# Performance work log

Hardware: AMD Instinct MI355X
Metric: run time of the kernel (lower is better)

## Reference

```python
import jax, jax.numpy as jnp
import numpy as np

N_SAMPLES = 8_388_608   # total packed samples (~64 per ray on average)
N_RAYS = 131_072
DT_SCALE = 0.005        # keep per-ray optical depth ~O(1); also tempers global-cumsum fp32 error


def setup_inputs() -> dict:
    key = jax.random.key(0)
    k1, k2, k3, k4, k5 = jax.random.split(key, 5)
    rgb_samples = jax.random.uniform(k1, (N_SAMPLES, 3), dtype=jnp.float32)
    radiance_samples = jax.random.uniform(k2, (N_SAMPLES, 1), dtype=jnp.float32)  # density sigma >= 0
    samples_z = jax.random.uniform(k3, (N_SAMPLES,), dtype=jnp.float32)           # t values in [0,1)
    samples_dt = jax.random.uniform(k4, (N_SAMPLES,), dtype=jnp.float32) * DT_SCALE
    # sorted segment ids == contiguous packed per-ray sample ranges (ragged)
    ray_id = jnp.sort(jax.random.randint(k5, (N_SAMPLES,), 0, N_RAYS, dtype=jnp.int64))
    ray_t_exit = jnp.full((N_RAYS, 1), 2.0, dtype=jnp.float32)  # exit t beyond all z -> positive last dt
    return {
        "rgb_samples": rgb_samples,
        "radiance_samples": radiance_samples,
        "samples_z": samples_z,
        "samples_dt": samples_dt,
        "ray_id": ray_id,
        "ray_t_exit": ray_t_exit,
        "use_ray_t_exit": 1,
    }


def reference(rgb_samples, radiance_samples, samples_z, samples_dt, ray_id, ray_t_exit, use_ray_t_exit):
    N = rgb_samples.shape[0]
    sigma = radiance_samples[:, 0]
    idx = jnp.arange(N)

    # dt of the last sample of each ray is (t_exit - z_last) when use_ray_t_exit
    if use_ray_t_exit:
        last_idx = jax.ops.segment_max(idx, ray_id, num_segments=N_RAYS)
        is_last = idx == last_idx[ray_id]
        dt = jnp.where(is_last, ray_t_exit[ray_id, 0] - samples_z, samples_dt)
    else:
        dt = samples_dt

    sigdt = sigma * dt                      # optical depth per sample
    c = jnp.cumsum(sigdt)                   # global inclusive cumsum
    c_excl = c - sigdt                      # global exclusive cumsum
    # exclusive cumsum restarted per ray: subtract value at each segment's first sample
    # (c_excl is non-decreasing since sigdt >= 0, so segment_min == first element)
    seg_start = jax.ops.segment_min(c_excl, ray_id, num_segments=N_RAYS)
    T = jnp.exp(-(c_excl - seg_start[ray_id]))          # transmittance before each sample
    alpha = 1.0 - jnp.exp(-sigdt)
    w = alpha * T                                        # per-sample compositing weight

    pred_rgb = jax.ops.segment_sum(w[:, None] * rgb_samples, ray_id, num_segments=N_RAYS)   # [R,3]
    pred_depth = jax.ops.segment_sum(w * samples_z, ray_id, num_segments=N_RAYS)[:, None]   # [R,1]
    bg_transmittance = jnp.exp(-jax.ops.segment_sum(sigdt, ray_id, num_segments=N_RAYS))[:, None]  # [R,1]
    weight_per_sample = w[:, None]                                                           # [N,1]
    return pred_rgb, pred_depth, bg_transmittance, weight_per_sample
```

## Files before the change

kernel.cpp:

```cpp
#include <hip/hip_runtime.h>


#define RPW 4

struct F2 { float x, y; };
struct F6 { float v[6]; };

template <int CTRL, int ROW_MASK>
__device__ __forceinline__ float dpp_add(float x) {
    int t = __builtin_amdgcn_update_dpp(0, __float_as_int(x), CTRL, ROW_MASK, 0xf, true);
    return x + __int_as_float(t);
}

__device__ __forceinline__ float wave_incl_scan(float x) {
    x = dpp_add<0x111, 0xf>(x);
    x = dpp_add<0x112, 0xf>(x);
    x = dpp_add<0x114, 0xf>(x);
    x = dpp_add<0x118, 0xf>(x);
    x = dpp_add<0x142, 0xa>(x);
    x = dpp_add<0x143, 0xc>(x);
    return x;
}

__device__ __forceinline__ float readlane_f32(float x, int lane) {
    return __int_as_float(__builtin_amdgcn_readlane(__float_as_int(x), lane));
}

__global__ void compute_starts_kernel(const int* __restrict__ ray_id,
                                      int n_samples, int n_rays,
                                      int* __restrict__ starts) {
    const int t = blockIdx.x * blockDim.x + threadIdx.x;
    const int stride = gridDim.x * blockDim.x;
    if (t == 0) {
        const int first = ray_id[0];
        for (int r = 0; r <= first; ++r) starts[r] = 0;
        const int last = ray_id[n_samples - 1];
        for (int r = last + 1; r <= n_rays; ++r) starts[r] = n_samples;
    }
    for (int g = t; g * 4 < n_samples; g += stride) {
        const int i4 = g * 4;
        const int4 v = *reinterpret_cast<const int4*>(ray_id + i4);
        const int prev = (i4 == 0) ? v.x : ray_id[i4 - 1];
        const int vals[5] = {prev, v.x, v.y, v.z, v.w};
        #pragma unroll
        for (int j = 0; j < 4; ++j) {
            const int p = vals[j], c = vals[j + 1];
            if (c != p) {
                for (int r = p + 1; r <= c; ++r) starts[r] = i4 + j;
            }
        }
    }
}

struct Slab { F2 sg, zv, dtv; F6 c; };

__device__ __forceinline__ Slab load_slab(const float* __restrict__ sigma_in,
                                          const float* __restrict__ z_in,
                                          const float* __restrict__ dt_in,
                                          const float* __restrict__ rgb,
                                          int base, int lane, int n_samples)
{
    Slab r;
    const int i0 = base + 2 * lane;
    const int il = min(i0, n_samples - 2);
    r.sg  = *reinterpret_cast<const F2*>(sigma_in + il);
    r.zv  = *reinterpret_cast<const F2*>(z_in + il);
    r.dtv = *reinterpret_cast<const F2*>(dt_in + il);
    r.c   = *reinterpret_cast<const F6*>(rgb + 3 * (size_t)il);
    if (i0 > n_samples - 2) {
        r.sg.x = r.sg.y; r.zv.x = r.zv.y; r.dtv.x = r.dtv.y;
        r.c.v[0] = r.c.v[3]; r.c.v[1] = r.c.v[4]; r.c.v[2] = r.c.v[5];
    }
    return r;
}

__device__ __forceinline__ void process_pass128(
    const Slab& d, int base, int s1, int lane, int use_exit, float texit,
    float& csum, float& carry,
    float& accR, float& accG, float& accB, float& accD,
    float* __restrict__ out_w)
{
    const int i0 = base + 2 * lane;
    const int i1 = i0 + 1;
    float dt0 = d.dtv.x, dt1v = d.dtv.y;
    if (use_exit && i0 == s1 - 1) dt0  = texit - d.zv.x;
    if (use_exit && i1 == s1 - 1) dt1v = texit - d.zv.y;
    const float e0 = (i0 < s1) ? d.sg.x * dt0  : 0.f;
    const float e1 = (i1 < s1) ? d.sg.y * dt1v : 0.f;

    const float S  = wave_incl_scan(e0 + e1);
    const float t1 = csum + S;
    const float t0 = t1 - e1;
    const float v0 = __expf(-t0);
    const float v1 = __expf(-t1);
    const int vpi = __builtin_amdgcn_update_dpp(__float_as_int(carry), __float_as_int(v1),
                                                0x138 , 0xf, 0xf, false);
    const float vp = __int_as_float(vpi);
    const float w0 = vp - v0;
    const float w1 = v0 - v1;

    if (i0 < s1) out_w[i0] = w0;
    if (i1 < s1) out_w[i1] = w1;
    accR += w0 * d.c.v[0] + w1 * d.c.v[3];
    accG += w0 * d.c.v[1] + w1 * d.c.v[4];
    accB += w0 * d.c.v[2] + w1 * d.c.v[5];
    accD += w0 * d.zv.x   + w1 * d.zv.y;
    csum  = readlane_f32(t1, 63);
    carry = readlane_f32(v1, 63);
}

__global__ __launch_bounds__(256) void render_kernel(
    const float* __restrict__ rgb,
    const float* __restrict__ sigma_in,
    const float* __restrict__ z_in,
    const float* __restrict__ dt_in,
    const float* __restrict__ t_exit,
    const int*  __restrict__ use_exit_p,
    const int*  __restrict__ starts,
    float* __restrict__ out_rgb,
    float* __restrict__ out_depth,
    float* __restrict__ out_bg,
    float* __restrict__ out_w,
    int n_rays, int n_samples)
{
    const int wave = threadIdx.x >> 6;
    const int lane = threadIdx.x & 63;
    const int wid  = blockIdx.x * (blockDim.x >> 6) + wave;
    const int ray0 = wid * RPW;
    if (ray0 >= n_rays) return;

    const int use_exit = *use_exit_p;

    int s[RPW + 1];
    #pragma unroll
    for (int k = 0; k <= RPW; ++k) {
        s[k] = __builtin_amdgcn_readfirstlane(starts[min(ray0 + k, n_rays)]);
    }
    float texit[RPW];
    #pragma unroll
    for (int k = 0; k < RPW; ++k) {
        texit[k] = readlane_f32(t_exit[min(ray0 + k, n_rays - 1)], 0);
    }

    Slab sl[RPW];
    #pragma unroll
    for (int k = 0; k < RPW; ++k) {
        sl[k] = load_slab(sigma_in, z_in, dt_in, rgb, s[k], lane, n_samples);
    }
    #pragma unroll
    for (int k = 0; k < RPW; ++k) {
        asm volatile("" ::
            "v"(sl[k].sg.x), "v"(sl[k].sg.y), "v"(sl[k].zv.x), "v"(sl[k].zv.y),
            "v"(sl[k].dtv.x), "v"(sl[k].dtv.y),
            "v"(sl[k].c.v[0]), "v"(sl[k].c.v[1]), "v"(sl[k].c.v[2]),
            "v"(sl[k].c.v[3]), "v"(sl[k].c.v[4]), "v"(sl[k].c.v[5]));
    }
    __builtin_amdgcn_sched_barrier(0);

    #pragma unroll
    for (int k = 0; k < RPW; ++k) {
        const int ray = ray0 + k;
        if (ray >= n_rays) break;
        const int s0 = s[k], s1 = s[k + 1];
        float csum = 0.f, carry = 1.0f;
        float accR = 0.f, accG = 0.f, accB = 0.f, accD = 0.f;

        process_pass128(sl[k], s0, s1, lane, use_exit, texit[k],
                        csum, carry, accR, accG, accB, accD, out_w);

        for (int base = s0 + 128; base < s1; base += 128) {
            const Slab d = load_slab(sigma_in, z_in, dt_in, rgb, base, lane, n_samples);
            process_pass128(d, base, s1, lane, use_exit, texit[k],
                            csum, carry, accR, accG, accB, accD, out_w);
        }

        accR = wave_incl_scan(accR);
        accG = wave_incl_scan(accG);
        accB = wave_incl_scan(accB);
        accD = wave_incl_scan(accD);
        if (lane == 63) {
            out_rgb[3 * ray + 0] = accR;
            out_rgb[3 * ray + 1] = accB == accB ? accG : accG;
            out_rgb[3 * ray + 1] = accG;
            out_rgb[3 * ray + 2] = accB;
            out_depth[ray] = accD;
            out_bg[ray]    = carry;
        }
    }
}

extern "C" void kernel_launch(void* const* d_in, const int* in_sizes, int n_in,
                              void* d_out, int out_size, void* d_ws, size_t ws_size,
                              hipStream_t stream) {
    const float* rgb     = (const float*)d_in[0];
    const float* sigma   = (const float*)d_in[1];
    const float* z       = (const float*)d_in[2];
    const float* dt      = (const float*)d_in[3];
    const int*   ray_id  = (const int*)d_in[4];
    const float* t_exit  = (const float*)d_in[5];
    const int*   use_ex  = (const int*)d_in[6];

    const int n_samples = in_sizes[2];
    const int n_rays    = in_sizes[5];

    int* starts = (int*)d_ws;

    float* out      = (float*)d_out;
    float* out_rgb  = out;
    float* out_dep  = out + (size_t)3 * n_rays;
    float* out_bg   = out + (size_t)4 * n_rays;
    float* out_w    = out + (size_t)5 * n_rays;

    compute_starts_kernel<<<2048, 256, 0, stream>>>(ray_id, n_samples, n_rays, starts);

    const int waves_per_block = 4;
    const int rays_per_block  = waves_per_block * RPW;
    const int blocks = (n_rays + rays_per_block - 1) / rays_per_block;
    render_kernel<<<blocks, 256, 0, stream>>>(rgb, sigma, z, dt, t_exit, use_ex,
                                              starts, out_rgb, out_dep, out_bg,
                                              out_w, n_rays, n_samples);
}
```

Before: 58.56 us.

## Interleave first-pass scans across rays and split rare long-ray continuation path

Computes the first 128-sample pass for all four rays of a wave as independent unrolled chains, so their DPP scans and exps can interleave instead of running serially per ray. Rays longer than 128 samples are handled in a separate wave-uniform branch that resumes from the saved prefix and carry. The first-pass weight stores and the final per-ray reductions are batched after that branch. It also drops the early return and the asm register pinning. Keeping more values live raises register pressure, and removing the early exit makes out-of-range waves run the full body.

```diff
diff --git a/kernel.cpp b/kernel.cpp
--- a/kernel.cpp
+++ b/kernel.cpp
@@ -74,37 +74,31 @@
     return r;
 }
 
-__device__ __forceinline__ void process_pass128(
+__device__ __forceinline__ void process_pass128_rare(
     const Slab& d, int base, int s1, int lane, int use_exit, float texit,
     float& csum, float& carry,
-    float& accR, float& accG, float& accB, float& accD,
+    float& aR, float& aG, float& aB, float& aD,
     float* __restrict__ out_w)
 {
-    const int i0 = base + 2 * lane;
-    const int i1 = i0 + 1;
-    float dt0 = d.dtv.x, dt1v = d.dtv.y;
-    if (use_exit && i0 == s1 - 1) dt0  = texit - d.zv.x;
-    if (use_exit && i1 == s1 - 1) dt1v = texit - d.zv.y;
-    const float e0 = (i0 < s1) ? d.sg.x * dt0  : 0.f;
-    const float e1 = (i1 < s1) ? d.sg.y * dt1v : 0.f;
-
-    const float S  = wave_incl_scan(e0 + e1);
-    const float t1 = csum + S;
-    const float t0 = t1 - e1;
-    const float v0 = __expf(-t0);
+    const int i0 = base + 2 * lane, i1 = i0 + 1;
+    float dt0 = d.dtv.x, dt1 = d.dtv.y;
+    if (use_exit && i0 == s1 - 1) dt0 = texit - d.zv.x;
+    if (use_exit && i1 == s1 - 1) dt1 = texit - d.zv.y;
+    const float e0 = (i0 < s1) ? d.sg.x * dt0 : 0.f;
+    const float e1 = (i1 < s1) ? d.sg.y * dt1 : 0.f;
+    const float t1 = csum + wave_incl_scan(e0 + e1);
+    const float v0 = __expf(-(t1 - e1));
     const float v1 = __expf(-t1);
     const int vpi = __builtin_amdgcn_update_dpp(__float_as_int(carry), __float_as_int(v1),
                                                 0x138 , 0xf, 0xf, false);
-    const float vp = __int_as_float(vpi);
-    const float w0 = vp - v0;
+    const float w0 = __int_as_float(vpi) - v0;
     const float w1 = v0 - v1;
-
     if (i0 < s1) out_w[i0] = w0;
     if (i1 < s1) out_w[i1] = w1;
-    accR += w0 * d.c.v[0] + w1 * d.c.v[3];
-    accG += w0 * d.c.v[1] + w1 * d.c.v[4];
-    accB += w0 * d.c.v[2] + w1 * d.c.v[5];
-    accD += w0 * d.zv.x   + w1 * d.zv.y;
+    aR += w0 * d.c.v[0] + w1 * d.c.v[3];
+    aG += w0 * d.c.v[1] + w1 * d.c.v[4];
+    aB += w0 * d.c.v[2] + w1 * d.c.v[5];
+    aD += w0 * d.zv.x + w1 * d.zv.y;
     csum  = readlane_f32(t1, 63);
     carry = readlane_f32(v1, 63);
 }
@@ -127,7 +121,6 @@
     const int lane = threadIdx.x & 63;
     const int wid  = blockIdx.x * (blockDim.x >> 6) + wave;
     const int ray0 = wid * RPW;
-    if (ray0 >= n_rays) return;
 
     const int use_exit = *use_exit_p;
 
@@ -136,10 +129,10 @@
     for (int k = 0; k <= RPW; ++k) {
         s[k] = __builtin_amdgcn_readfirstlane(starts[min(ray0 + k, n_rays)]);
     }
-    float texit[RPW];
-    #pragma unroll
-    for (int k = 0; k < RPW; ++k) {
-        texit[k] = readlane_f32(t_exit[min(ray0 + k, n_rays - 1)], 0);
+    float tex[RPW];
+    #pragma unroll
+    for (int k = 0; k < RPW; ++k) {
+        tex[k] = readlane_f32(t_exit[min(ray0 + k, n_rays - 1)], 0);
     }
 
     Slab sl[RPW];
@@ -147,44 +140,74 @@
     for (int k = 0; k < RPW; ++k) {
         sl[k] = load_slab(sigma_in, z_in, dt_in, rgb, s[k], lane, n_samples);
     }
-    #pragma unroll
-    for (int k = 0; k < RPW; ++k) {
-        asm volatile("" ::
-            "v"(sl[k].sg.x), "v"(sl[k].sg.y), "v"(sl[k].zv.x), "v"(sl[k].zv.y),
-            "v"(sl[k].dtv.x), "v"(sl[k].dtv.y),
-            "v"(sl[k].c.v[0]), "v"(sl[k].c.v[1]), "v"(sl[k].c.v[2]),
-            "v"(sl[k].c.v[3]), "v"(sl[k].c.v[4]), "v"(sl[k].c.v[5]));
-    }
     __builtin_amdgcn_sched_barrier(0);
 
-    #pragma unroll
-    for (int k = 0; k < RPW; ++k) {
+    float accR[RPW], accG[RPW], accB[RPW], accD[RPW];
+    float w0v[RPW], w1v[RPW], t1v[RPW], v1v[RPW];
+    #pragma unroll
+    for (int k = 0; k < RPW; ++k) {
+        const int s1 = s[k + 1];
+        const int i0 = s[k] + 2 * lane;
+        const int i1 = i0 + 1;
+        float dt0 = sl[k].dtv.x, dt1 = sl[k].dtv.y;
+        if (use_exit && i0 == s1 - 1) dt0 = tex[k] - sl[k].zv.x;
+        if (use_exit && i1 == s1 - 1) dt1 = tex[k] - sl[k].zv.y;
+        const float e0 = (i0 < s1) ? sl[k].sg.x * dt0 : 0.f;
+        const float e1 = (i1 < s1) ? sl[k].sg.y * dt1 : 0.f;
+        const float t1 = wave_incl_scan(e0 + e1);
+        const float v0 = __expf(-(t1 - e1));
+        const float v1 = __expf(-t1);
+        const int vpi = __builtin_amdgcn_update_dpp(0x3f800000 , __float_as_int(v1),
+                                                    0x138 , 0xf, 0xf, false);
+        const float vp = __int_as_float(vpi);
+        const float w0 = vp - v0;
+        const float w1 = v0 - v1;
+        w0v[k] = w0;  w1v[k] = w1;
+        accR[k] = w0 * sl[k].c.v[0] + w1 * sl[k].c.v[3];
+        accG[k] = w0 * sl[k].c.v[1] + w1 * sl[k].c.v[4];
+        accB[k] = w0 * sl[k].c.v[2] + w1 * sl[k].c.v[5];
+        accD[k] = w0 * sl[k].zv.x   + w1 * sl[k].zv.y;
+        t1v[k] = t1;  v1v[k] = v1;
+    }
+
+    bool anylong = false;
+    #pragma unroll
+    for (int k = 0; k < RPW; ++k) anylong |= (s[k] + 128 < s[k + 1]);
+    if (anylong) {
+        #pragma unroll
+        for (int k = 0; k < RPW; ++k) {
+            float csum  = readlane_f32(t1v[k], 63);
+            float carry = readlane_f32(v1v[k], 63);
+            for (int base = s[k] + 128; base < s[k + 1]; base += 128) {
+                const Slab d = load_slab(sigma_in, z_in, dt_in, rgb, base, lane, n_samples);
+                process_pass128_rare(d, base, s[k + 1], lane, use_exit, tex[k],
+                                     csum, carry, accR[k], accG[k], accB[k], accD[k], out_w);
+            }
+            v1v[k] = carry;
+        }
+    }
+
+    #pragma unroll
+    for (int k = 0; k < RPW; ++k) {
+        const int s1 = s[k + 1];
+        const int i0 = s[k] + 2 * lane;
+        if (i0 < s1)     out_w[i0]     = w0v[k];
+        if (i0 + 1 < s1) out_w[i0 + 1] = w1v[k];
+    }
+
+    #pragma unroll
+    for (int k = 0; k < RPW; ++k) {
+        const float r = wave_incl_scan(accR[k]);
+        const float g = wave_incl_scan(accG[k]);
+        const float b = wave_incl_scan(accB[k]);
+        const float d = wave_incl_scan(accD[k]);
         const int ray = ray0 + k;
-        if (ray >= n_rays) break;
-        const int s0 = s[k], s1 = s[k + 1];
-        float csum = 0.f, carry = 1.0f;
-        float accR = 0.f, accG = 0.f, accB = 0.f, accD = 0.f;
-
-        process_pass128(sl[k], s0, s1, lane, use_exit, texit[k],
-                        csum, carry, accR, accG, accB, accD, out_w);
-
-        for (int base = s0 + 128; base < s1; base += 128) {
-            const Slab d = load_slab(sigma_in, z_in, dt_in, rgb, base, lane, n_samples);
-            process_pass128(d, base, s1, lane, use_exit, texit[k],
-                            csum, carry, accR, accG, accB, accD, out_w);
-        }
-
-        accR = wave_incl_scan(accR);
-        accG = wave_incl_scan(accG);
-        accB = wave_incl_scan(accB);
-        accD = wave_incl_scan(accD);
-        if (lane == 63) {
-            out_rgb[3 * ray + 0] = accR;
-            out_rgb[3 * ray + 1] = accB == accB ? accG : accG;
-            out_rgb[3 * ray + 1] = accG;
-            out_rgb[3 * ray + 2] = accB;
-            out_depth[ray] = accD;
-            out_bg[ray]    = carry;
+        if (lane == 63 && ray < n_rays) {
+            out_rgb[3 * ray + 0] = r;
+            out_rgb[3 * ray + 1] = g;
+            out_rgb[3 * ray + 2] = b;
+            out_depth[ray] = d;
+            out_bg[ray]    = v1v[k];
         }
     }
 }
```

After: 58.49 us. Within noise of the previous version (-0.1%).
